# Kernel optimization log

Hardware: AMD Instinct MI355X
Metric: run time of the kernel (lower is better)

## Reference

```python
import jax, jax.numpy as jnp
import numpy as np

NEG = -1000000000.0

def setup_inputs() -> dict:
    key = jax.random.key(0)
    k1, k2, k3, k4 = jax.random.split(key, 4)
    B, Sq, Sk, D = 8, 2048, 2048, 1024
    query = jax.random.normal(k1, (B, Sq, D), dtype=jnp.float32)
    memories = jax.random.normal(k2, (B, Sk, D), dtype=jnp.float32)
    mask = jax.random.randint(k3, (B, Sq, Sk), 0, 2).astype(jnp.int32)
    W = jax.random.normal(k4, (D, D), dtype=jnp.float32) * (1.0 / np.sqrt(D))
    b = jnp.zeros((D,), dtype=jnp.float32)
    return {"query": query, "memories": memories, "mask": mask, "W": W, "b": b}

def reference(query, memories, mask, W, b):
    # linear projection: nn.Linear applies x @ W^T + b
    q = jnp.einsum('bsd,od->bso', query, W) + b
    add_mask = (1.0 - mask.astype(q.dtype)) * NEG
    # [B,Sq,Sk] attention logits
    attn_logits = jnp.einsum('bqd,bkd->bqk', q, memories) + add_mask
    attn_weights = jax.nn.softmax(attn_logits, axis=-1)
    attn_outputs = jnp.einsum('bqk,bkd->bqd', attn_weights, memories)
    return attn_outputs
```

## Files before the change

### kernel.cpp

```cpp
#include <hip/hip_runtime.h>


typedef __attribute__((ext_vector_type(8))) _Float16 f16x8;
typedef __attribute__((ext_vector_type(4))) float f32x4;
typedef unsigned short u16;
typedef unsigned int u32;

#define B_ 8
#define SQL 2048
#define SKL 2048
#define DD 1024
#define NEGC -1000000000.0f

static __device__ __forceinline__ u16 f2h(float x) {
  _Float16 h = (_Float16)x;
  return __builtin_bit_cast(u16, h);
}
static __device__ __forceinline__ float h2f(u16 v) {
  return (float)__builtin_bit_cast(_Float16, v);
}
static __device__ __forceinline__ void gload16(const void* g, void* l) {
  __builtin_amdgcn_global_load_lds((const __attribute__((address_space(1))) u32*)g,
                                   (__attribute__((address_space(3))) u32*)l, 16, 0, 0);
}

__global__ __launch_bounds__(256) void prep_k(const float* __restrict__ query,
                                              u16* __restrict__ q16,
                                              const float* __restrict__ Wm,
                                              u16* __restrict__ wh, u16* __restrict__ wl) {
  if (blockIdx.x < 2048) {
    long n = (long)B_ * SQL * DD;
    long i = ((long)blockIdx.x * 256 + threadIdx.x) * 8;
    long stride = 2048L * 256 * 8;
    for (; i < n; i += stride) {
      float4 v0 = *(const float4*)(query + i);
      float4 v1 = *(const float4*)(query + i + 4);
      ushort4 o0 = make_ushort4(f2h(v0.x), f2h(v0.y), f2h(v0.z), f2h(v0.w));
      ushort4 o1 = make_ushort4(f2h(v1.x), f2h(v1.y), f2h(v1.z), f2h(v1.w));
      *(ushort4*)(q16 + i) = o0;
      *(ushort4*)(q16 + i + 4) = o1;
    }
  } else {
    long i = ((long)(blockIdx.x - 2048) * 256 + threadIdx.x) * 8;
    float4 v0 = *(const float4*)(Wm + i);
    float4 v1 = *(const float4*)(Wm + i + 4);
    u16 h0 = f2h(v0.x), h1 = f2h(v0.y), h2 = f2h(v0.z), h3 = f2h(v0.w);
    u16 h4 = f2h(v1.x), h5 = f2h(v1.y), h6 = f2h(v1.z), h7 = f2h(v1.w);
    *(ushort4*)(wh + i) = make_ushort4(h0, h1, h2, h3);
    *(ushort4*)(wh + i + 4) = make_ushort4(h4, h5, h6, h7);
    *(ushort4*)(wl + i) = make_ushort4(f2h(v0.x - h2f(h0)), f2h(v0.y - h2f(h1)),
                                       f2h(v0.z - h2f(h2)), f2h(v0.w - h2f(h3)));
    *(ushort4*)(wl + i + 4) = make_ushort4(f2h(v1.x - h2f(h4)), f2h(v1.y - h2f(h5)),
                                           f2h(v1.z - h2f(h6)), f2h(v1.w - h2f(h7)));
  }
}

__global__ __launch_bounds__(256, 2) void proj_split_k(
    const u16* __restrict__ Ah, const u16* __restrict__ Bh, const u16* __restrict__ Bl,
    const float* __restrict__ bias, u16* __restrict__ C0,
    const float* __restrict__ mem, u16* __restrict__ memh, u16* __restrict__ memT) {
  __shared__ u16 lA[256 * 64];
  __shared__ u16 lB[128 * 128];

  if (blockIdx.x < 512) {
    const int N = DD, K = DD;
    int id = blockIdx.x;
    int j = (id & 7) * 64 + (id >> 3);
    const int TX = N >> 7;
    const int by = j / TX, bx = j % TX;
    const int tid = threadIdx.x;
    const int l = tid & 63, w = tid >> 6;
    const int wr = w >> 1, wc = w & 1;
    const long am0 = (long)by * 256;
    const long bn0 = (long)bx * 128;

    f32x4 acc[8][4];
#pragma unroll
    for (int i = 0; i < 8; ++i)
#pragma unroll
      for (int j2 = 0; j2 < 4; ++j2) {
        f32x4 z = {0.f, 0.f, 0.f, 0.f};
        acc[i][j2] = z;
      }
    const int lrow = l & 15, lch = l >> 4;

    for (int k0 = 0; k0 < K; k0 += 64) {
      __syncthreads();
#pragma unroll
      for (int i = 0; i < 8; ++i) {
        int row = i * 32 + (tid >> 3);
        int cc = (tid & 7) ^ (row & 7);
        gload16(Ah + (am0 + row) * K + k0 + cc * 8, &lA[row * 64 + (tid & 7) * 8]);
      }
#pragma unroll
      for (int i = 0; i < 8; ++i) {
        int row = i * 16 + (tid >> 4);
        int s = tid & 15;
        int cc = s ^ (row & 15);
        const u16* src = (cc < 8) ? (Bh + (bn0 + row) * K + k0 + cc * 8)
                                  : (Bl + (bn0 + row) * K + k0 + (cc - 8) * 8);
        gload16(src, &lB[row * 128 + s * 8]);
      }
      __syncthreads();

#pragma unroll
      for (int kk = 0; kk < 2; ++kk) {
        f16x8 ah[8], bh[4], bl_[4];
#pragma unroll
        for (int f = 0; f < 8; ++f) {
          int ra = wr * 128 + f * 16 + lrow;
          int c = kk * 4 + lch;
          ah[f] = *(const f16x8*)&lA[ra * 64 + (c ^ (ra & 7)) * 8];
        }
#pragma unroll
        for (int f = 0; f < 4; ++f) {
          int rb = wc * 64 + f * 16 + lrow;
          int c = kk * 4 + lch;
          bh[f] = *(const f16x8*)&lB[rb * 128 + (c ^ (rb & 15)) * 8];
          bl_[f] = *(const f16x8*)&lB[rb * 128 + ((8 + c) ^ (rb & 15)) * 8];
        }
#pragma unroll
        for (int mf = 0; mf < 8; ++mf)
#pragma unroll
          for (int nf = 0; nf < 4; ++nf) {
            acc[mf][nf] = __builtin_amdgcn_mfma_f32_16x16x32_f16(ah[mf], bh[nf], acc[mf][nf], 0, 0, 0);
            acc[mf][nf] = __builtin_amdgcn_mfma_f32_16x16x32_f16(ah[mf], bl_[nf], acc[mf][nf], 0, 0, 0);
          }
      }
    }
#pragma unroll
    for (int mf = 0; mf < 8; ++mf)
#pragma unroll
      for (int nf = 0; nf < 4; ++nf)
#pragma unroll
        for (int r = 0; r < 4; ++r) {
          long row = am0 + wr * 128 + mf * 16 + (l >> 4) * 4 + r;
          long col = bn0 + wc * 64 + nf * 16 + (l & 15);
          C0[row * N + col] = f2h(acc[mf][nf][r] + bias[col]);
        }
  } else {
    u16(*t)[65] = (u16(*)[65])lA;
    int id2 = blockIdx.x - 512;
    int bx = id2 & 15, by = (id2 >> 4) & 31, bz = id2 >> 9;
    long bo = (long)bz * SKL * DD;
    int r0 = by * 64, c0 = bx * 64;
    int tr = threadIdx.x / 16, tc4 = (threadIdx.x % 16) * 4;
#pragma unroll
    for (int i = 0; i < 4; ++i) {
      int r = tr + i * 16;
      long idx = bo + (long)(r0 + r) * DD + c0 + tc4;
      float4 v = *(const float4*)(mem + idx);
      u16 h0 = f2h(v.x), h1 = f2h(v.y), h2 = f2h(v.z), h3 = f2h(v.w);
      *(ushort4*)(memh + idx) = make_ushort4(h0, h1, h2, h3);
      t[r][tc4 + 0] = h0; t[r][tc4 + 1] = h1; t[r][tc4 + 2] = h2; t[r][tc4 + 3] = h3;
    }
    __syncthreads();
#pragma unroll
    for (int i = 0; i < 4; ++i) {
      int c = tr + i * 16;
      ushort4 v = make_ushort4(t[tc4 + 0][c], t[tc4 + 1][c], t[tc4 + 2][c], t[tc4 + 3][c]);
      *(ushort4*)(memT + bo + (long)(c0 + c) * SKL + r0 + tc4) = v;
    }
  }
}

template <int OUTMODE>
__global__ __launch_bounds__(512, 2) void gemm8_f16(
    const u16* __restrict__ Ah, const u16* __restrict__ Bh,
    void* __restrict__ C0,
    int N, int K, int TPB, long batchA, long batchB, long batchC) {
  __shared__ u16 lA[2][256 * 64];
  __shared__ u16 lB[2][256 * 64];

  const int nwg = gridDim.x;
  int id = blockIdx.x;
  int j = (id & 7) * (nwg >> 3) + (id >> 3);
  const int TX = N >> 8;
  const int bz = j / TPB;
  const int r0_ = j % TPB;
  const int by = r0_ / TX, bx = r0_ % TX;

  const u16* pA = Ah + (long)bz * batchA;
  const u16* pB = Bh + (long)bz * batchB;

  const int tid = threadIdx.x;
  const int l = tid & 63, w = tid >> 6;
  const int wr = w >> 2, wc = w & 3;
  const long am0 = (long)by * 256;
  const long bn0 = (long)bx * 256;
  const int lrow = l & 15, lch = l >> 4;
  const int srow = tid >> 3, schunk = tid & 7;

  f32x4 acc[8][4];
#pragma unroll
  for (int i = 0; i < 8; ++i)
#pragma unroll
    for (int j2 = 0; j2 < 4; ++j2) {
      f32x4 z = {0.f, 0.f, 0.f, 0.f};
      acc[i][j2] = z;
    }

  auto STAGE_HALF = [&](int buf, int isB, int half, int k0) {
    const u16* p = isB ? pB : pA;
    long b0 = isB ? bn0 : am0;
    u16* dst = isB ? &lB[buf][0] : &lA[buf][0];
#pragma unroll
    for (int i = 0; i < 2; ++i) {
      int row = half * 128 + i * 64 + srow;
      int cc = schunk ^ (row & 7);
      gload16(p + (b0 + row) * K + k0 + cc * 8, dst + row * 64 + schunk * 8);
    }
  };

  STAGE_HALF(0, 0, 0, 0); STAGE_HALF(0, 0, 1, 0);
  STAGE_HALF(0, 1, 0, 0); STAGE_HALF(0, 1, 1, 0);
  asm volatile("s_waitcnt vmcnt(0)" ::: "memory");
  __builtin_amdgcn_sched_barrier(0);
  __builtin_amdgcn_s_barrier();

  const int KITER = K >> 6;
  for (int t = 0; t < KITER; ++t) {
    const int c = t & 1;
    const int k1 = (t + 1) << 6;
    const bool more = (t + 1 < KITER);

    f16x8 bfr[4][2];
#pragma unroll
    for (int nf = 0; nf < 4; ++nf)
#pragma unroll
      for (int kk = 0; kk < 2; ++kk) {
        int rb = wc * 64 + nf * 16 + lrow;
        int cch = kk * 4 + lch;
        bfr[nf][kk] = *(const f16x8*)&lB[c][rb * 64 + (cch ^ (rb & 7)) * 8];
      }

#pragma unroll
    for (int p = 0; p < 4; ++p) {
      f16x8 afr[2][2];
#pragma unroll
      for (int mi = 0; mi < 2; ++mi)
#pragma unroll
        for (int kk = 0; kk < 2; ++kk) {
          int ra = wr * 128 + (2 * p + mi) * 16 + lrow;
          int cch = kk * 4 + lch;
          afr[mi][kk] = *(const f16x8*)&lA[c][ra * 64 + (cch ^ (ra & 7)) * 8];
        }
      if (more) {
        if (p == 0)      STAGE_HALF(c ^ 1, 0, 0, k1);
        else if (p == 1) STAGE_HALF(c ^ 1, 0, 1, k1);
        else if (p == 2) STAGE_HALF(c ^ 1, 1, 0, k1);
        else             STAGE_HALF(c ^ 1, 1, 1, k1);
      }
      __builtin_amdgcn_s_barrier();
      __builtin_amdgcn_s_setprio(1);
#pragma unroll
      for (int kk = 0; kk < 2; ++kk)
#pragma unroll
        for (int mi = 0; mi < 2; ++mi)
#pragma unroll
          for (int nf = 0; nf < 4; ++nf)
            acc[2 * p + mi][nf] = __builtin_amdgcn_mfma_f32_16x16x32_f16(
                afr[mi][kk], bfr[nf][kk], acc[2 * p + mi][nf], 0, 0, 0);
      __builtin_amdgcn_s_setprio(0);
      __builtin_amdgcn_s_barrier();
    }

    if (more) {
      asm volatile("s_waitcnt vmcnt(0)" ::: "memory");
      __builtin_amdgcn_sched_barrier(0);
      __builtin_amdgcn_s_barrier();
    }
  }

#pragma unroll
  for (int mf = 0; mf < 8; ++mf)
#pragma unroll
    for (int nf = 0; nf < 4; ++nf)
#pragma unroll
      for (int r = 0; r < 4; ++r) {
        long row = am0 + wr * 128 + mf * 16 + (l >> 4) * 4 + r;
        long col = bn0 + wc * 64 + nf * 16 + (l & 15);
        long idx = (long)bz * batchC + row * N + col;
        if (OUTMODE == 0) ((float*)C0)[idx] = acc[mf][nf][r];
        else              ((u16*)C0)[idx] = f2h(acc[mf][nf][r]);
      }
}

__global__ __launch_bounds__(256) void softmax16_k(const float* __restrict__ S,
                                                   const int* __restrict__ M,
                                                   u16* __restrict__ P) {
  long row = (long)blockIdx.x * 4 + (threadIdx.x >> 6);
  const float* s = S + row * SKL;
  const int* m = M + row * SKL;
  u16* p = P + row * SKL;
  const int lane = threadIdx.x & 63;
  float x[32];
#pragma unroll
  for (int j = 0; j < 8; ++j) {
    float4 v = *(const float4*)(s + lane * 4 + j * 256);
    int4 q = *(const int4*)(m + lane * 4 + j * 256);
    x[j * 4 + 0] = q.x ? v.x : v.x + NEGC;
    x[j * 4 + 1] = q.y ? v.y : v.y + NEGC;
    x[j * 4 + 2] = q.z ? v.z : v.z + NEGC;
    x[j * 4 + 3] = q.w ? v.w : v.w + NEGC;
  }
  float mx = x[0];
#pragma unroll
  for (int j = 1; j < 32; ++j) mx = fmaxf(mx, x[j]);
#pragma unroll
  for (int o = 32; o >= 1; o >>= 1) mx = fmaxf(mx, __shfl_xor(mx, o, 64));
  float sum = 0.f;
#pragma unroll
  for (int j = 0; j < 32; ++j) { x[j] = __expf(x[j] - mx); sum += x[j]; }
#pragma unroll
  for (int o = 32; o >= 1; o >>= 1) sum += __shfl_xor(sum, o, 64);
  float inv = 1.f / sum;
#pragma unroll
  for (int j = 0; j < 8; ++j) {
    ushort4 o4 = make_ushort4(f2h(x[j * 4 + 0] * inv), f2h(x[j * 4 + 1] * inv),
                              f2h(x[j * 4 + 2] * inv), f2h(x[j * 4 + 3] * inv));
    *(ushort4*)(p + lane * 4 + j * 256) = o4;
  }
}

extern "C" void kernel_launch(void* const* d_in, const int* in_sizes, int n_in,
                              void* d_out, int out_size, void* d_ws, size_t ws_size,
                              hipStream_t stream) {
  const float* query = (const float*)d_in[0];
  const float* mem = (const float*)d_in[1];
  const int* mask = (const int*)d_in[2];
  const float* Wm = (const float*)d_in[3];
  const float* bias = (const float*)d_in[4];
  float* out = (float*)d_out;

  const long nQ = (long)B_ * SQL * DD;
  const long nW = (long)DD * DD;
  const long nS = (long)B_ * SQL * SKL;

  char* ws = (char*)d_ws;
  u16* q16 = (u16*)ws; ws += nQ * 2;
  u16* memh = (u16*)ws; ws += nQ * 2;
  u16* memT = (u16*)ws; ws += nQ * 2;
  u16* q1 = (u16*)ws; ws += nQ * 2;
  u16* wh = (u16*)ws; ws += nW * 2;
  u16* wl = (u16*)ws; ws += nW * 2;
  float* S = (float*)ws; ws += nS * 4;
  u16* P = q16;

  prep_k<<<2048 + 512, 256, 0, stream>>>(query, q16, Wm, wh, wl);
  proj_split_k<<<512 + 4096, 256, 0, stream>>>(q16, wh, wl, bias, q1, mem, memh, memT);
  gemm8_f16<0><<<512, 512, 0, stream>>>(
      q1, memh, S, SKL, DD, 64,
      (long)SQL * DD, (long)SKL * DD, (long)SQL * SKL);
  softmax16_k<<<(B_ * SQL) / 4, 256, 0, stream>>>(S, mask, P);
  gemm8_f16<0><<<256, 512, 0, stream>>>(
      P, memT, out, DD, SKL, 32,
      (long)SQL * SKL, (long)DD * SKL, (long)SQL * DD);
}
```

Baseline: 339.4 us.

## Split GEMM staging waits so compute starts before all tile loads land

Loads for the next K-tile are reordered so B and the interleaved A row blocks arrive in the order they are consumed. The single end-of-iteration full vmcnt(0) wait is replaced by a partial vmcnt(2) wait at loop top and a vmcnt(4) wait before the second half of the A fragments. MFMA work on early rows can then begin while the remaining A rows are still in flight, which removes part of the pipeline bubble. The cost is more fragile hand-counted waitcnt logic tied to the exact number of issued loads.

```diff
diff --git a/kernel.cpp b/kernel.cpp
--- a/kernel.cpp
+++ b/kernel.cpp
@@ -165,7 +165,7 @@
 }
 
 template <int OUTMODE>
-__global__ __launch_bounds__(512, 2) void gemm8_f16(
+__global__ __launch_bounds__(512, 2) void gemm8p_f16(
     const u16* __restrict__ Ah, const u16* __restrict__ Bh,
     void* __restrict__ C0,
     int N, int K, int TPB, long batchA, long batchB, long batchC) {
@@ -200,29 +200,32 @@
       acc[i][j2] = z;
     }
 
-  auto STAGE_HALF = [&](int buf, int isB, int half, int k0) {
-    const u16* p = isB ? pB : pA;
-    long b0 = isB ? bn0 : am0;
-    u16* dst = isB ? &lB[buf][0] : &lA[buf][0];
-#pragma unroll
-    for (int i = 0; i < 2; ++i) {
-      int row = half * 128 + i * 64 + srow;
-      int cc = schunk ^ (row & 7);
-      gload16(p + (b0 + row) * K + k0 + cc * 8, dst + row * 64 + schunk * 8);
-    }
+  auto LD64 = [&](const u16* p, long b0, u16* dst, int rbase, int k0) {
+    int row = rbase + srow;
+    int cc = schunk ^ (row & 7);
+    gload16(p + (b0 + row) * K + k0 + cc * 8, dst + row * 64 + schunk * 8);
   };
 
-  STAGE_HALF(0, 0, 0, 0); STAGE_HALF(0, 0, 1, 0);
-  STAGE_HALF(0, 1, 0, 0); STAGE_HALF(0, 1, 1, 0);
-  asm volatile("s_waitcnt vmcnt(0)" ::: "memory");
-  __builtin_amdgcn_sched_barrier(0);
-  __builtin_amdgcn_s_barrier();
+  {
+    u16* dA = &lA[0][0];
+    u16* dB = &lB[0][0];
+    LD64(pB, bn0, dB, 0, 0);   LD64(pB, bn0, dB, 64, 0);
+    LD64(pB, bn0, dB, 128, 0); LD64(pB, bn0, dB, 192, 0);
+    LD64(pA, am0, dA, 0, 0);   LD64(pA, am0, dA, 128, 0);
+    LD64(pA, am0, dA, 64, 0);  LD64(pA, am0, dA, 192, 0);
+  }
 
   const int KITER = K >> 6;
   for (int t = 0; t < KITER; ++t) {
     const int c = t & 1;
     const int k1 = (t + 1) << 6;
     const bool more = (t + 1 < KITER);
+    u16* dA = &lA[c ^ 1][0];
+    u16* dB = &lB[c ^ 1][0];
+
+    asm volatile("s_waitcnt vmcnt(2)" ::: "memory");
+    __builtin_amdgcn_sched_barrier(0);
+    __builtin_amdgcn_s_barrier();
 
     f16x8 bfr[4][2];
 #pragma unroll
@@ -236,6 +239,12 @@
 
 #pragma unroll
     for (int p = 0; p < 4; ++p) {
+      if (p == 2) {
+        if (more) asm volatile("s_waitcnt vmcnt(4)" ::: "memory");
+        else      asm volatile("s_waitcnt vmcnt(0)" ::: "memory");
+        __builtin_amdgcn_sched_barrier(0);
+        __builtin_amdgcn_s_barrier();
+      }
       f16x8 afr[2][2];
 #pragma unroll
       for (int mi = 0; mi < 2; ++mi)
@@ -246,10 +255,10 @@
           afr[mi][kk] = *(const f16x8*)&lA[c][ra * 64 + (cch ^ (ra & 7)) * 8];
         }
       if (more) {
-        if (p == 0)      STAGE_HALF(c ^ 1, 0, 0, k1);
-        else if (p == 1) STAGE_HALF(c ^ 1, 0, 1, k1);
-        else if (p == 2) STAGE_HALF(c ^ 1, 1, 0, k1);
-        else             STAGE_HALF(c ^ 1, 1, 1, k1);
+        if (p == 0)      { LD64(pB, bn0, dB, 0, k1);   LD64(pB, bn0, dB, 64, k1); }
+        else if (p == 1) { LD64(pB, bn0, dB, 128, k1); LD64(pB, bn0, dB, 192, k1); }
+        else if (p == 2) { LD64(pA, am0, dA, 0, k1);   LD64(pA, am0, dA, 128, k1); }
+        else             { LD64(pA, am0, dA, 64, k1);  LD64(pA, am0, dA, 192, k1); }
       }
       __builtin_amdgcn_s_barrier();
       __builtin_amdgcn_s_setprio(1);
@@ -262,12 +271,6 @@
             acc[2 * p + mi][nf] = __builtin_amdgcn_mfma_f32_16x16x32_f16(
                 afr[mi][kk], bfr[nf][kk], acc[2 * p + mi][nf], 0, 0, 0);
       __builtin_amdgcn_s_setprio(0);
-      __builtin_amdgcn_s_barrier();
-    }
-
-    if (more) {
-      asm volatile("s_waitcnt vmcnt(0)" ::: "memory");
-      __builtin_amdgcn_sched_barrier(0);
       __builtin_amdgcn_s_barrier();
     }
   }
@@ -349,11 +352,11 @@
 
   prep_k<<<2048 + 512, 256, 0, stream>>>(query, q16, Wm, wh, wl);
   proj_split_k<<<512 + 4096, 256, 0, stream>>>(q16, wh, wl, bias, q1, mem, memh, memT);
-  gemm8_f16<0><<<512, 512, 0, stream>>>(
+  gemm8p_f16<0><<<512, 512, 0, stream>>>(
       q1, memh, S, SKL, DD, 64,
       (long)SQL * DD, (long)SKL * DD, (long)SQL * SKL);
   softmax16_k<<<(B_ * SQL) / 4, 256, 0, stream>>>(S, mask, P);
-  gemm8_f16<0><<<256, 512, 0, stream>>>(
+  gemm8p_f16<0><<<256, 512, 0, stream>>>(
       P, memT, out, DD, SKL, 32,
       (long)SQL * SKL, (long)DD * SKL, (long)SQL * DD);
 }
```

After: 331.8 us. 1.02x faster.
